# Optimization experiments

Hardware: AMD Instinct MI355X
Metric: run time of the kernel (lower is better)

Reference implementation:

```python
import jax, jax.numpy as jnp
import numpy as np

B, N, D = 2, 2048, 1024
CTX, TV = 256, 250
H, DH = 16, 64
INNER = H * DH          # 1024
FF = 4 * D              # 4096 (GEGLU inner)
SCALE = DH ** -0.5


def _layernorm(x, g, b):
    mu = x.mean(-1, keepdims=True)
    var = ((x - mu) ** 2).mean(-1, keepdims=True)
    return (x - mu) / jnp.sqrt(var + 1e-5) * g + b


def _attn(xq, ctx, wq, wk, wv, wo, bo):
    b, n, _ = xq.shape
    m = ctx.shape[1]
    q = (xq @ wq).reshape(b, n, H, DH)
    k = (ctx @ wk).reshape(b, m, H, DH)
    v = (ctx @ wv).reshape(b, m, H, DH)
    sim = jnp.einsum('bihd,bjhd->bhij', q, k) * SCALE
    att = jax.nn.softmax(sim, axis=-1)
    out = jnp.einsum('bhij,bjhd->bihd', att, v).reshape(b, n, INNER)
    return out @ wo + bo


def _sin_pe(T, d):
    pos = jnp.arange(T, dtype=jnp.float32)[:, None]
    den = jnp.power(10000.0, 2.0 * jnp.arange(d // 2, dtype=jnp.float32) / d)
    ang = pos / den                                  # [T, d/2]
    return jnp.stack([jnp.sin(ang), jnp.cos(ang)], -1).reshape(T, d)


def setup_inputs() -> dict:
    key = jax.random.key(0)
    ks = jax.random.split(key, 40)
    w = lambda k, s: jax.random.normal(k, s, jnp.float32) * 0.02
    inp = {
        'x': jax.random.normal(ks[0], (B, N, D), jnp.float32),
        'context': jax.random.normal(ks[1], (B, CTX, D), jnp.float32),
        'hint_control': jax.random.normal(ks[2], (B, TV, D), jnp.float32),
        'ln1_g': jnp.ones((D,)), 'ln1_b': jnp.zeros((D,)),
        'ln2_g': jnp.ones((D,)), 'ln2_b': jnp.zeros((D,)),
        'ln3_g': jnp.ones((D,)), 'ln3_b': jnp.zeros((D,)),
        'ln4_g': jnp.ones((D,)), 'ln4_b': jnp.zeros((D,)),
        'a1_wq': w(ks[3], (D, INNER)), 'a1_wk': w(ks[4], (D, INNER)),
        'a1_wv': w(ks[5], (D, INNER)), 'a1_wo': w(ks[6], (INNER, D)),
        'a1_bo': jnp.zeros((D,)),
        'a2_wq': w(ks[7], (D, INNER)), 'a2_wk': w(ks[8], (D, INNER)),
        'a2_wv': w(ks[9], (D, INNER)), 'a2_wo': w(ks[10], (INNER, D)),
        'a2_bo': jnp.zeros((D,)),
        'a3_wq': w(ks[11], (D, INNER)), 'a3_wk': w(ks[12], (D, INNER)),
        'a3_wv': w(ks[13], (D, INNER)), 'a3_wo': w(ks[14], (INNER, D)),
        'a3_bo': jnp.zeros((D,)),
        'ff_w1': w(ks[15], (D, 2 * FF)), 'ff_b1': jnp.zeros((2 * FF,)),
        'ff_w2': w(ks[16], (FF, D)), 'ff_b2': jnp.zeros((D,)),
    }
    return inp


def reference(x, context, hint_control,
              ln1_g, ln1_b, ln2_g, ln2_b, ln3_g, ln3_b, ln4_g, ln4_b,
              a1_wq, a1_wk, a1_wv, a1_wo, a1_bo,
              a2_wq, a2_wk, a2_wv, a2_wo, a2_bo,
              a3_wq, a3_wk, a3_wv, a3_wo, a3_bo,
              ff_w1, ff_b1, ff_w2, ff_b2):
    # attn1: self-attention (disable_self_attn=False -> context is x itself)
    h = _layernorm(x, ln1_g, ln1_b)
    x = _attn(h, h, a1_wq, a1_wk, a1_wv, a1_wo, a1_bo) + x
    # attn2: cross-attention over context
    h = _layernorm(x, ln2_g, ln2_b)
    x = _attn(h, context, a2_wq, a2_wk, a2_wv, a2_wo, a2_bo) + x
    # attn3: video cross-attention with sinusoidal PE added to hint_control
    hint = hint_control + _sin_pe(hint_control.shape[1], D)[None]
    h = _layernorm(x, ln4_g, ln4_b)
    x = _attn(h, hint, a3_wq, a3_wk, a3_wv, a3_wo, a3_bo) + x
    # GEGLU feed-forward
    h = _layernorm(x, ln3_g, ln3_b)
    proj = h @ ff_w1 + ff_b1
    a, gate = jnp.split(proj, 2, axis=-1)
    x = (a * jax.nn.gelu(gate, approximate=False)) @ ff_w2 + ff_b2 + x
    return x
```

## Files before the change

kernel.cpp:

```cpp
#include <hip/hip_runtime.h>
#include <cstdint>

typedef unsigned short u16;
typedef __bf16 bf16x8 __attribute__((ext_vector_type(8)));
typedef float f32x4 __attribute__((ext_vector_type(4)));

__device__ __forceinline__ u16 f2bf(float f) {
  union { float f; uint32_t u; } x; x.f = f;
  uint32_t r = x.u + 0x7FFFu + ((x.u >> 16) & 1u);
  return (u16)(r >> 16);
}
__device__ __forceinline__ bf16x8 ld8s(const u16* p) {
  return *reinterpret_cast<const bf16x8*>(p);
}
__device__ __forceinline__ float geluf(float x) {
  return 0.5f * x * (1.f + erff(x * 0.70710678118654752f));
}
__device__ __forceinline__ uint32_t cvtpk(float a, float b) {
  uint32_t r;
  asm("v_cvt_pk_bf16_f32 %0, %1, %2" : "=v"(r) : "v"(a), "v"(b));
  return r;
}
__device__ __forceinline__ void gload16(const u16* g, u16* l) {
  __builtin_amdgcn_global_load_lds(
      (__attribute__((address_space(1))) void*)const_cast<u16*>(g),
      (__attribute__((address_space(3))) void*)l, 16, 0, 0);
}

struct PrepJob {
  const void* src; void* dst;
  int K, N, mode, row_off, ldo, s_lo, s_hi, blk0;
};
struct PrepArgs { PrepJob j[17]; };

__global__ __launch_bounds__(256) void wprep_kernel(PrepArgs a) {
  __shared__ float tile[32][33];
  int bid = blockIdx.x;
  int t = threadIdx.x;
  const float* src = nullptr; void* dst = nullptr;
  int K = 0, N = 0, mode = 0, roff = 0, ldo = 0, slo = 0, shi = 0, bl = 0;
#pragma unroll
  for (int i = 0; i < 17; ++i) {
    int lo = a.j[i].blk0;
    int hi = (i == 16) ? 0x7fffffff : a.j[i + 1].blk0;
    if (bid >= lo && bid < hi) {
      src = (const float*)a.j[i].src; dst = a.j[i].dst;
      K = a.j[i].K; N = a.j[i].N; mode = a.j[i].mode; roff = a.j[i].row_off;
      ldo = a.j[i].ldo; slo = a.j[i].s_lo; shi = a.j[i].s_hi; bl = bid - lo;
    }
  }
  (void)K;
  if (mode <= 1) {
    int nb = N >> 5;
    int bx = bl % nb, by = bl / nb;
    int tx = t & 31, ty = t >> 5;
    int n = bx * 32 + tx, kbase = by * 32;
#pragma unroll
    for (int r = 0; r < 4; ++r)
      tile[ty + r * 8][tx] = src[(size_t)(kbase + ty + r * 8) * N + n];
    __syncthreads();
#pragma unroll
    for (int r = 0; r < 4; ++r) {
      int nl = ty + r * 8, ng = bx * 32 + nl;
      int orow;
      if (mode == 0) orow = roff + ng;
      else {
        if (ng < 4096) orow = ((ng >> 4) << 5) + (ng & 15);
        else { int t2 = ng - 4096; orow = ((t2 >> 4) << 5) + 16 + (t2 & 15); }
      }
      float v = tile[tx][nl];
      if (mode == 0 && orow >= slo && orow < shi) v *= 0.18033688011112042f;
      ((u16*)dst)[(size_t)orow * ldo + kbase + tx] = f2bf(v);
    }
  } else if (mode == 2) {
    int idx = bl * 1024 + t * 4;
    float4 v = *reinterpret_cast<const float4*>(src + idx);
    ushort4 o;
    o.x = f2bf(v.x); o.y = f2bf(v.y); o.z = f2bf(v.z); o.w = f2bf(v.w);
    *reinterpret_cast<ushort4*>((u16*)dst + idx) = o;
  } else if (mode == 3) {
    int row = bl;
    int tt = row % 250;
    int d0 = t * 4;
    int i0 = d0 >> 1;
    float den0 = powf(10000.f, (float)i0 / 512.f);
    float den1 = powf(10000.f, (float)(i0 + 1) / 512.f);
    float a0 = (float)tt / den0, a1 = (float)tt / den1;
    const float* hp = src + (size_t)row * 1024 + d0;
    u16* op = (u16*)dst + (size_t)row * 1024 + d0;
    op[0] = f2bf(hp[0] + sinf(a0));
    op[1] = f2bf(hp[1] + cosf(a0));
    op[2] = f2bf(hp[2] + sinf(a1));
    op[3] = f2bf(hp[3] + cosf(a1));
  } else {
    int i2 = bl * 256 + t;
    int g = i2 >> 5, s2 = i2 & 31;
    int c2 = (s2 < 16) ? (g * 16 + s2) : (4096 + g * 16 + (s2 - 16));
    ((float*)dst)[i2] = src[c2];
  }
}

__global__ __launch_bounds__(256) void ln_kernel(const float* __restrict__ x,
                                                 const float* __restrict__ g,
                                                 const float* __restrict__ b,
                                                 u16* __restrict__ out) {
  int row = blockIdx.x;
  int tid = threadIdx.x;
  int l = tid & 63, w = tid >> 6;
  const float4 v = reinterpret_cast<const float4*>(x + (size_t)row * 1024)[tid];
  float s = v.x + v.y + v.z + v.w;
#pragma unroll
  for (int d = 1; d < 64; d <<= 1) s += __shfl_xor(s, d, 64);
  __shared__ float red[8];
  if (l == 0) red[w] = s;
  __syncthreads();
  float mean = (red[0] + red[1] + red[2] + red[3]) * (1.f / 1024.f);
  float dx = v.x - mean, dy = v.y - mean, dz = v.z - mean, dw = v.w - mean;
  float vs = dx * dx + dy * dy + dz * dz + dw * dw;
#pragma unroll
  for (int d = 1; d < 64; d <<= 1) vs += __shfl_xor(vs, d, 64);
  if (l == 0) red[4 + w] = vs;
  __syncthreads();
  float var = (red[4] + red[5] + red[6] + red[7]) * (1.f / 1024.f);
  float rstd = rsqrtf(var + 1e-5f);
  const float4 g4 = reinterpret_cast<const float4*>(g)[tid];
  const float4 b4 = reinterpret_cast<const float4*>(b)[tid];
  ushort4 o;
  o.x = f2bf(dx * rstd * g4.x + b4.x);
  o.y = f2bf(dy * rstd * g4.y + b4.y);
  o.z = f2bf(dz * rstd * g4.z + b4.z);
  o.w = f2bf(dw * rstd * g4.w + b4.w);
  reinterpret_cast<ushort4*>(out + (size_t)row * 1024)[tid] = o;
}

template <int EPI, bool GUARD>
__global__ __launch_bounds__(256) void gemm_bt_kernel(
    const u16* __restrict__ A, int lda, const u16* __restrict__ Bt,
    void* __restrict__ Cv, int ldc, const float* __restrict__ bias,
    const float* __restrict__ res, int M, int N, int K) {
  __shared__ __align__(16) u16 As[128 * 64];
  __shared__ __align__(16) u16 Bs[128 * 64];
  int t = threadIdx.x;
  int l = t & 63, w = t >> 6;
  int wm = w >> 1, wn = w & 1;
  int lr = l & 15, lg = l >> 4;
  int gx = gridDim.x;
  int nwg = gx * gridDim.y;
  int orig = blockIdx.y * gx + blockIdx.x;
  int qq = nwg >> 3, rr = nwg & 7;
  int xcd = orig & 7, lin = orig >> 3;
  int wg = (xcd < rr ? xcd * (qq + 1) : rr * (qq + 1) + (xcd - rr) * qq) + lin;
  int bx = wg % gx, by = wg / gx;
  int row0 = by * 128, n0 = bx * 128;

  int lrow8 = l >> 3, lchunk = l & 7;
  f32x4 acc[4][4];
#pragma unroll
  for (int i = 0; i < 4; ++i)
#pragma unroll
    for (int j = 0; j < 4; ++j) acc[i][j] = f32x4{0.f, 0.f, 0.f, 0.f};

  int keyA = lr & 7;
  for (int k0 = 0; k0 < K; k0 += 64) {
#pragma unroll
    for (int q = 0; q < 4; ++q) {
      int rbase = w * 32 + q * 8;
      int r = rbase + lrow8;
      int csrc = (lchunk ^ lrow8) * 8;
      int ga = row0 + r;
      if (GUARD) { if (ga > M - 1) ga = M - 1; }
      gload16(&A[(size_t)ga * lda + k0 + csrc], &As[rbase * 64]);
      int gb = n0 + r;
      gload16(&Bt[(size_t)gb * K + k0 + csrc], &Bs[rbase * 64]);
    }
    __syncthreads();
#pragma unroll
    for (int kk = 0; kk < 2; ++kk) {
      bf16x8 af[4], bfv[4];
#pragma unroll
      for (int mi = 0; mi < 4; ++mi)
        af[mi] = ld8s(&As[(wm * 64 + mi * 16 + lr) * 64 + ((((kk << 2) + lg) ^ keyA) << 3)]);
#pragma unroll
      for (int ni = 0; ni < 4; ++ni)
        bfv[ni] = ld8s(&Bs[(wn * 64 + ni * 16 + lr) * 64 + ((((kk << 2) + lg) ^ keyA) << 3)]);
#pragma unroll
      for (int mi = 0; mi < 4; ++mi)
#pragma unroll
        for (int ni = 0; ni < 4; ++ni)
          acc[mi][ni] = __builtin_amdgcn_mfma_f32_16x16x32_bf16(af[mi], bfv[ni], acc[mi][ni], 0, 0, 0);
    }
    __syncthreads();
  }

#pragma unroll
  for (int mi = 0; mi < 4; ++mi) {
    int rowb = row0 + wm * 64 + mi * 16 + lg * 4;
    if (EPI == 2) {
#pragma unroll
      for (int p = 0; p < 2; ++p) {
        int colA = n0 + wn * 64 + p * 32 + lr;
        int colG = colA + 16;
        int ocol = ((n0 + wn * 64) >> 1) + p * 16 + lr;
#pragma unroll
        for (int r = 0; r < 4; ++r) {
          int grow = rowb + r;
          float av = acc[mi][2 * p][r] + bias[colA];
          float gv = acc[mi][2 * p + 1][r] + bias[colG];
          ((u16*)Cv)[(size_t)grow * ldc + ocol] = f2bf(av * geluf(gv));
        }
      }
    } else {
#pragma unroll
      for (int ni = 0; ni < 4; ++ni) {
        int gcol = n0 + wn * 64 + ni * 16 + lr;
#pragma unroll
        for (int r = 0; r < 4; ++r) {
          int grow = rowb + r;
          if (GUARD && grow >= M) continue;
          float v = acc[mi][ni][r];
          if (EPI == 0)
            ((u16*)Cv)[(size_t)grow * ldc + gcol] = f2bf(v);
          else
            ((float*)Cv)[(size_t)grow * ldc + gcol] =
                v + bias[gcol] + res[(size_t)grow * ldc + gcol];
        }
      }
    }
  }
}

template <bool TG>
__global__ __launch_bounds__(256) void attn_kernel(
    const u16* __restrict__ Q, int qs, int qoff,
    const u16* __restrict__ KV, int kvs, int koff, int voff,
    int m, u16* __restrict__ O) {
  int b = blockIdx.z, h = blockIdx.y;
  int t = threadIdx.x;
  int l = t & 63, w = t >> 6;
  int lr = l & 15, lg = l >> 4;
  int q0 = blockIdx.x * 128 + w * 16;
  __shared__ __align__(16) u16 Ks[2][64 * 64];
  __shared__ __align__(16) u16 Vt[2][64 * 64];
  __shared__ __align__(16) u16 Pl[4][16 * 64];

  const u16* qrowA = Q + (size_t)((b << 11) + q0 + lr) * qs + qoff + h * 64;
  const u16* qrowB = qrowA + (size_t)64 * qs;
  bf16x8 qa0 = ld8s(qrowA + lg * 8), qa1 = ld8s(qrowA + 32 + lg * 8);
  bf16x8 qb0 = ld8s(qrowB + lg * 8), qb1 = ld8s(qrowB + 32 + lg * 8);

  f32x4 oA[4], oB[4];
  float psA = 0.f, psB = 0.f;
#pragma unroll
  for (int r = 0; r < 4; ++r) { oA[r] = f32x4{0.f, 0.f, 0.f, 0.f}; oB[r] = f32x4{0.f, 0.f, 0.f, 0.f}; }

  const u16* kvb = KV + (size_t)b * m * kvs + h * 64;
  int kj = t >> 3, kc = t & 7;
  int srcsw = ((l & 7) ^ (l >> 3)) << 3;
  int psw = (lr & 7) ^ ((lr & 8) >> 1);

  {
#pragma unroll
    for (int q2 = 0; q2 < 2; ++q2) {
      int gr = w * 16 + q2 * 8 + (l >> 3);
      if (TG) { if (gr > m - 1) gr = m - 1; }
      gload16(kvb + (size_t)gr * kvs + koff + srcsw, &Ks[0][(w * 16 + q2 * 8) * 64]);
    }
    int jv = kj * 2;
    int gv0 = jv, gv1 = jv + 1;
    if (TG) { if (gv0 > m - 1) gv0 = m - 1; if (gv1 > m - 1) gv1 = m - 1; }
    uint4 va = *reinterpret_cast<const uint4*>(kvb + (size_t)gv0 * kvs + voff + kc * 8);
    uint4 vb2 = *reinterpret_cast<const uint4*>(kvb + (size_t)gv1 * kvs + voff + kc * 8);
    const u16* vap = reinterpret_cast<const u16*>(&va);
    const u16* vbp = reinterpret_cast<const u16*>(&vb2);
    int jb = jv >> 3, jlow = jv & 7;
#pragma unroll
    for (int i = 0; i < 8; ++i) {
      int d = kc * 8 + i;
      int key = (d ^ (d >> 3)) & 7;
      uint32_t pk = (uint32_t)vap[i] | ((uint32_t)vbp[i] << 16);
      *reinterpret_cast<uint32_t*>(&Vt[0][d * 64 + ((jb ^ key) << 3) + jlow]) = pk;
    }
  }
  __syncthreads();

  int nj = (m + 63) >> 6;
  int cur = 0;
  for (int jt = 0; jt < nj; ++jt) {
    int j0 = jt << 6;
    bool hn = (jt + 1 < nj);
    uint4 va, vb2;
    if (hn) {
      int j0n = j0 + 64;
#pragma unroll
      for (int q2 = 0; q2 < 2; ++q2) {
        int gr = j0n + w * 16 + q2 * 8 + (l >> 3);
        if (TG) { if (gr > m - 1) gr = m - 1; }
        gload16(kvb + (size_t)gr * kvs + koff + srcsw, &Ks[cur ^ 1][(w * 16 + q2 * 8) * 64]);
      }
      int jv = kj * 2;
      int gv0 = j0n + jv, gv1 = j0n + jv + 1;
      if (TG) { if (gv0 > m - 1) gv0 = m - 1; if (gv1 > m - 1) gv1 = m - 1; }
      va = *reinterpret_cast<const uint4*>(kvb + (size_t)gv0 * kvs + voff + kc * 8);
      vb2 = *reinterpret_cast<const uint4*>(kvb + (size_t)gv1 * kvs + voff + kc * 8);
    }

    const u16* Kb = Ks[cur];
    f32x4 sA[4], sB[4];
#pragma unroll
    for (int c = 0; c < 4; ++c) {
      sA[c] = f32x4{0.f, 0.f, 0.f, 0.f};
      sB[c] = f32x4{0.f, 0.f, 0.f, 0.f};
      bf16x8 k0 = ld8s(&Kb[(c * 16 + lr) * 64 + ((lg ^ (lr & 7)) << 3)]);
      bf16x8 k1 = ld8s(&Kb[(c * 16 + lr) * 64 + (((4 + lg) ^ (lr & 7)) << 3)]);
      sA[c] = __builtin_amdgcn_mfma_f32_16x16x32_bf16(k0, qa0, sA[c], 0, 0, 0);
      sA[c] = __builtin_amdgcn_mfma_f32_16x16x32_bf16(k1, qa1, sA[c], 0, 0, 0);
      sB[c] = __builtin_amdgcn_mfma_f32_16x16x32_bf16(k0, qb0, sB[c], 0, 0, 0);
      sB[c] = __builtin_amdgcn_mfma_f32_16x16x32_bf16(k1, qb1, sB[c], 0, 0, 0);
    }

    if (hn) {
      const u16* vap = reinterpret_cast<const u16*>(&va);
      const u16* vbp = reinterpret_cast<const u16*>(&vb2);
      int jv = kj * 2;
      int jb = jv >> 3, jlow = jv & 7;
#pragma unroll
      for (int i = 0; i < 8; ++i) {
        int d = kc * 8 + i;
        int key = (d ^ (d >> 3)) & 7;
        uint32_t pk = (uint32_t)vap[i] | ((uint32_t)vbp[i] << 16);
        *reinterpret_cast<uint32_t*>(&Vt[cur ^ 1][d * 64 + ((jb ^ key) << 3) + jlow]) = pk;
      }
    }

    bool tail = TG && (j0 + 64 > m);
    const u16* Vb = Vt[cur];
    bf16x8 vfr[2][4];

    {
      uint32_t pk[8];
#pragma unroll
      for (int c = 0; c < 4; ++c) {
        float p[4];
#pragma unroll
        for (int r = 0; r < 4; ++r) {
          float v = exp2f(sA[c][r]);
          if (tail && (j0 + c * 16 + lg * 4 + r >= m)) v = 0.f;
          p[r] = v; psA += v;
        }
        pk[2 * c] = cvtpk(p[0], p[1]);
        pk[2 * c + 1] = cvtpk(p[2], p[3]);
      }
#pragma unroll
      for (int c = 0; c < 4; ++c) {
        int phys = (2 * c + (lg >> 1)) ^ psw;
        uint2 u; u.x = pk[2 * c]; u.y = pk[2 * c + 1];
        *reinterpret_cast<uint2*>(&Pl[w][lr * 64 + (phys << 3) + ((lg & 1) << 2)]) = u;
      }
#pragma unroll
      for (int ks = 0; ks < 2; ++ks) {
        int physp = (ks * 4 + lg) ^ psw;
        bf16x8 pb = ld8s(&Pl[w][lr * 64 + (physp << 3)]);
#pragma unroll
        for (int dt = 0; dt < 4; ++dt) {
          int d = dt * 16 + lr;
          int key = (d ^ (d >> 3)) & 7;
          vfr[ks][dt] = ld8s(&Vb[d * 64 + ((((ks << 2) + lg) ^ key) << 3)]);
          oA[dt] = __builtin_amdgcn_mfma_f32_16x16x32_bf16(vfr[ks][dt], pb, oA[dt], 0, 0, 0);
        }
      }
    }
    {
      uint32_t pk[8];
#pragma unroll
      for (int c = 0; c < 4; ++c) {
        float p[4];
#pragma unroll
        for (int r = 0; r < 4; ++r) {
          float v = exp2f(sB[c][r]);
          if (tail && (j0 + c * 16 + lg * 4 + r >= m)) v = 0.f;
          p[r] = v; psB += v;
        }
        pk[2 * c] = cvtpk(p[0], p[1]);
        pk[2 * c + 1] = cvtpk(p[2], p[3]);
      }
#pragma unroll
      for (int c = 0; c < 4; ++c) {
        int phys = (2 * c + (lg >> 1)) ^ psw;
        uint2 u; u.x = pk[2 * c]; u.y = pk[2 * c + 1];
        *reinterpret_cast<uint2*>(&Pl[w][lr * 64 + (phys << 3) + ((lg & 1) << 2)]) = u;
      }
#pragma unroll
      for (int ks = 0; ks < 2; ++ks) {
        int physp = (ks * 4 + lg) ^ psw;
        bf16x8 pb = ld8s(&Pl[w][lr * 64 + (physp << 3)]);
#pragma unroll
        for (int dt = 0; dt < 4; ++dt)
          oB[dt] = __builtin_amdgcn_mfma_f32_16x16x32_bf16(vfr[ks][dt], pb, oB[dt], 0, 0, 0);
      }
    }
    __syncthreads();
    cur ^= 1;
  }

  psA += __shfl_xor(psA, 16, 64); psA += __shfl_xor(psA, 32, 64);
  psB += __shfl_xor(psB, 16, 64); psB += __shfl_xor(psB, 32, 64);
  float invA = 1.f / psA, invB = 1.f / psB;
  {
    int grow = (b << 11) + q0 + lr;
    u16* op = O + (size_t)grow * 1024 + h * 64 + lg * 4;
#pragma unroll
    for (int dt = 0; dt < 4; ++dt) {
      uint2 u;
      u.x = cvtpk(oA[dt][0] * invA, oA[dt][1] * invA);
      u.y = cvtpk(oA[dt][2] * invA, oA[dt][3] * invA);
      *reinterpret_cast<uint2*>(op + dt * 16) = u;
    }
    u16* op2 = op + (size_t)64 * 1024;
#pragma unroll
    for (int dt = 0; dt < 4; ++dt) {
      uint2 u;
      u.x = cvtpk(oB[dt][0] * invB, oB[dt][1] * invB);
      u.y = cvtpk(oB[dt][2] * invB, oB[dt][3] * invB);
      *reinterpret_cast<uint2*>(op2 + dt * 16) = u;
    }
  }
}

extern "C" void kernel_launch(void* const* d_in, const int* in_sizes, int n_in,
                              void* d_out, int out_size, void* d_ws, size_t ws_size,
                              hipStream_t stream) {
  const float* x_in = (const float*)d_in[0];
  const float* ctx_in = (const float*)d_in[1];
  const float* hint_in = (const float*)d_in[2];
  const float* ln1g = (const float*)d_in[3]; const float* ln1b = (const float*)d_in[4];
  const float* ln2g = (const float*)d_in[5]; const float* ln2b = (const float*)d_in[6];
  const float* ln3g = (const float*)d_in[7]; const float* ln3b = (const float*)d_in[8];
  const float* ln4g = (const float*)d_in[9]; const float* ln4b = (const float*)d_in[10];
  const float* a1wq = (const float*)d_in[11]; const float* a1wk = (const float*)d_in[12];
  const float* a1wv = (const float*)d_in[13]; const float* a1wo = (const float*)d_in[14];
  const float* a1bo = (const float*)d_in[15];
  const float* a2wq = (const float*)d_in[16]; const float* a2wk = (const float*)d_in[17];
  const float* a2wv = (const float*)d_in[18]; const float* a2wo = (const float*)d_in[19];
  const float* a2bo = (const float*)d_in[20];
  const float* a3wq = (const float*)d_in[21]; const float* a3wk = (const float*)d_in[22];
  const float* a3wv = (const float*)d_in[23]; const float* a3wo = (const float*)d_in[24];
  const float* a3bo = (const float*)d_in[25];
  const float* ffw1 = (const float*)d_in[26]; const float* ffb1 = (const float*)d_in[27];
  const float* ffw2 = (const float*)d_in[28]; const float* ffb2 = (const float*)d_in[29];

  char* wsb = (char*)d_ws;
  size_t off = 0;
  auto alloc = [&](size_t bytes) -> void* {
    void* p = wsb + off;
    off += (bytes + 255) & ~(size_t)255;
    return p;
  };
  u16* wqkv1t = (u16*)alloc(3072ull * 1024 * 2);
  u16* wo1t = (u16*)alloc(1024ull * 1024 * 2);
  u16* wq2t = (u16*)alloc(1024ull * 1024 * 2);
  u16* wkv2t = (u16*)alloc(2048ull * 1024 * 2);
  u16* wo2t = (u16*)alloc(1024ull * 1024 * 2);
  u16* wq3t = (u16*)alloc(1024ull * 1024 * 2);
  u16* wkv3t = (u16*)alloc(2048ull * 1024 * 2);
  u16* wo3t = (u16*)alloc(1024ull * 1024 * 2);
  u16* w1t = (u16*)alloc(8192ull * 1024 * 2);
  u16* w2t = (u16*)alloc(1024ull * 4096 * 2);
  float* b1p = (float*)alloc(8192ull * 4);
  u16* hintbf = (u16*)alloc(500ull * 1024 * 2);
  u16* ctxbf = (u16*)alloc(512ull * 1024 * 2);
  float* xbuf = (float*)alloc(4096ull * 1024 * 4);
  u16* hbf = (u16*)alloc(4096ull * 1024 * 2);
  u16* attnout = (u16*)alloc(4096ull * 1024 * 2);
  u16* qbuf = (u16*)alloc(4096ull * 1024 * 2);
  u16* kvbuf = (u16*)alloc(512ull * 2048 * 2);
  u16* qkv = (u16*)alloc(4096ull * 4096 * 2);
  u16* gbuf = qkv;

  PrepArgs pa;
  int bi = 0, bc = 0;
  auto addJ = [&](const void* s, void* d, int K, int N, int mode, int roff,
                  int ldo, int slo, int shi, int nblk) {
    pa.j[bi].src = s; pa.j[bi].dst = d; pa.j[bi].K = K; pa.j[bi].N = N;
    pa.j[bi].mode = mode; pa.j[bi].row_off = roff; pa.j[bi].ldo = ldo;
    pa.j[bi].s_lo = slo; pa.j[bi].s_hi = shi; pa.j[bi].blk0 = bc;
    bc += nblk; ++bi;
  };
  addJ(a1wq, wqkv1t, 1024, 1024, 0, 0, 1024, 0, 1024, 1024);
  addJ(a1wk, wqkv1t, 1024, 1024, 0, 1024, 1024, 0, 0, 1024);
  addJ(a1wv, wqkv1t, 1024, 1024, 0, 2048, 1024, 0, 0, 1024);
  addJ(a1wo, wo1t, 1024, 1024, 0, 0, 1024, 0, 0, 1024);
  addJ(a2wq, wq2t, 1024, 1024, 0, 0, 1024, 0, 1024, 1024);
  addJ(a2wk, wkv2t, 1024, 1024, 0, 0, 1024, 0, 0, 1024);
  addJ(a2wv, wkv2t, 1024, 1024, 0, 1024, 1024, 0, 0, 1024);
  addJ(a2wo, wo2t, 1024, 1024, 0, 0, 1024, 0, 0, 1024);
  addJ(a3wq, wq3t, 1024, 1024, 0, 0, 1024, 0, 1024, 1024);
  addJ(a3wk, wkv3t, 1024, 1024, 0, 0, 1024, 0, 0, 1024);
  addJ(a3wv, wkv3t, 1024, 1024, 0, 1024, 1024, 0, 0, 1024);
  addJ(a3wo, wo3t, 1024, 1024, 0, 0, 1024, 0, 0, 1024);
  addJ(ffw1, w1t, 1024, 8192, 1, 0, 1024, 0, 0, 8192);
  addJ(ffw2, w2t, 4096, 1024, 0, 0, 4096, 0, 0, 4096);
  addJ(ctx_in, ctxbf, 0, 0, 2, 0, 0, 0, 0, 512);
  addJ(hint_in, hintbf, 0, 0, 3, 0, 0, 0, 0, 500);
  addJ(ffb1, b1p, 0, 0, 4, 0, 0, 0, 0, 32);
  wprep_kernel<<<bc, 256, 0, stream>>>(pa);

  ln_kernel<<<4096, 256, 0, stream>>>(x_in, ln1g, ln1b, hbf);
  gemm_bt_kernel<0, false><<<dim3(24, 32), 256, 0, stream>>>(hbf, 1024, wqkv1t, qkv, 3072,
                                                             nullptr, nullptr, 4096, 3072, 1024);
  attn_kernel<false><<<dim3(16, 16, 2), 256, 0, stream>>>(qkv, 3072, 0, qkv, 3072, 1024, 2048,
                                                          2048, attnout);
  gemm_bt_kernel<1, false><<<dim3(8, 32), 256, 0, stream>>>(attnout, 1024, wo1t, xbuf, 1024,
                                                            a1bo, x_in, 4096, 1024, 1024);

  ln_kernel<<<4096, 256, 0, stream>>>(xbuf, ln2g, ln2b, hbf);
  gemm_bt_kernel<0, false><<<dim3(8, 32), 256, 0, stream>>>(hbf, 1024, wq2t, qbuf, 1024,
                                                            nullptr, nullptr, 4096, 1024, 1024);
  gemm_bt_kernel<0, false><<<dim3(16, 4), 256, 0, stream>>>(ctxbf, 1024, wkv2t, kvbuf, 2048,
                                                            nullptr, nullptr, 512, 2048, 1024);
  attn_kernel<false><<<dim3(16, 16, 2), 256, 0, stream>>>(qbuf, 1024, 0, kvbuf, 2048, 0, 1024,
                                                          256, attnout);
  gemm_bt_kernel<1, false><<<dim3(8, 32), 256, 0, stream>>>(attnout, 1024, wo2t, xbuf, 1024,
                                                            a2bo, xbuf, 4096, 1024, 1024);

  ln_kernel<<<4096, 256, 0, stream>>>(xbuf, ln4g, ln4b, hbf);
  gemm_bt_kernel<0, false><<<dim3(8, 32), 256, 0, stream>>>(hbf, 1024, wq3t, qbuf, 1024,
                                                            nullptr, nullptr, 4096, 1024, 1024);
  gemm_bt_kernel<0, true><<<dim3(16, 4), 256, 0, stream>>>(hintbf, 1024, wkv3t, kvbuf, 2048,
                                                           nullptr, nullptr, 500, 2048, 1024);
  attn_kernel<true><<<dim3(16, 16, 2), 256, 0, stream>>>(qbuf, 1024, 0, kvbuf, 2048, 0, 1024,
                                                         250, attnout);
  gemm_bt_kernel<1, false><<<dim3(8, 32), 256, 0, stream>>>(attnout, 1024, wo3t, xbuf, 1024,
                                                            a3bo, xbuf, 4096, 1024, 1024);

  ln_kernel<<<4096, 256, 0, stream>>>(xbuf, ln3g, ln3b, hbf);
  gemm_bt_kernel<2, false><<<dim3(64, 32), 256, 0, stream>>>(hbf, 1024, w1t, gbuf, 4096,
                                                             b1p, nullptr, 4096, 8192, 1024);
  gemm_bt_kernel<1, false><<<dim3(8, 32), 256, 0, stream>>>(gbuf, 4096, w2t, d_out, 1024,
                                                            ffb2, xbuf, 4096, 1024, 4096);
}
```

Baseline: 548.8 us.

## Add 256x256 double-buffered GEMM kernel for QKV and GEGLU projections

Introduces a new 512-thread GEMM kernel with 256x256 output tiles and double-buffered LDS staging. It replaces the 128x128 kernel for the two largest GEMMs, the fused QKV projection and the GEGLU up-projection. The larger tile raises arithmetic intensity per global load, and the double buffering overlaps the next tile's loads with MFMA work. The cost is 128 KB of LDS per block and heavy register pressure from 32 accumulators per thread, which may limit occupancy. QKV also becomes only 192 blocks, which can underfill the GPU.

```diff
diff --git a/kernel.cpp b/kernel.cpp
--- a/kernel.cpp
+++ b/kernel.cpp
@@ -131,6 +131,101 @@
   o.z = f2bf(dz * rstd * g4.z + b4.z);
   o.w = f2bf(dw * rstd * g4.w + b4.w);
   reinterpret_cast<ushort4*>(out + (size_t)row * 1024)[tid] = o;
+}
+
+template <int EPI>
+__global__ __launch_bounds__(512, 2) void gemm256_kernel(
+    const u16* __restrict__ A, int lda, const u16* __restrict__ Bt,
+    void* __restrict__ Cv, int ldc, const float* __restrict__ bias,
+    int M, int N, int K) {
+  __shared__ __align__(16) u16 As[2][256 * 64];
+  __shared__ __align__(16) u16 Bs[2][256 * 64];
+  int t = threadIdx.x;
+  int l = t & 63, w = t >> 6;
+  int wm = w >> 2, wn = w & 3;
+  int lr = l & 15, lg = l >> 4;
+  int gx = gridDim.x;
+  int nwg = gx * gridDim.y;
+  int orig = blockIdx.y * gx + blockIdx.x;
+  int qq = nwg >> 3, rr = nwg & 7;
+  int xcd = orig & 7, lin = orig >> 3;
+  int wg = (xcd < rr ? xcd * (qq + 1) : rr * (qq + 1) + (xcd - rr) * qq) + lin;
+  int bx = wg % gx, by = wg / gx;
+  int row0 = by * 256, n0 = bx * 256;
+
+  int lrow8 = l >> 3, lchunk = l & 7;
+  int csrc = (lchunk ^ lrow8) * 8;
+  int keyA = lr & 7;
+
+  f32x4 acc[8][4];
+#pragma unroll
+  for (int i = 0; i < 8; ++i)
+#pragma unroll
+    for (int j = 0; j < 4; ++j) acc[i][j] = f32x4{0.f, 0.f, 0.f, 0.f};
+
+  auto stage = [&](int buf, int k0) {
+#pragma unroll
+    for (int q = 0; q < 4; ++q) {
+      int rbase = w * 32 + q * 8;
+      int r = rbase + lrow8;
+      gload16(&A[(size_t)(row0 + r) * lda + k0 + csrc], &As[buf][rbase * 64]);
+      gload16(&Bt[(size_t)(n0 + r) * K + k0 + csrc], &Bs[buf][rbase * 64]);
+    }
+  };
+
+  int nk = K >> 6;
+  stage(0, 0);
+  __syncthreads();
+  int cur = 0;
+  for (int ti = 0; ti < nk; ++ti) {
+    if (ti + 1 < nk) stage(cur ^ 1, (ti + 1) << 6);
+#pragma unroll
+    for (int kk = 0; kk < 2; ++kk) {
+      int chunk = (((kk << 2) + lg) ^ keyA) << 3;
+      bf16x8 af[8];
+#pragma unroll
+      for (int mi = 0; mi < 8; ++mi)
+        af[mi] = ld8s(&As[cur][(wm * 128 + mi * 16 + lr) * 64 + chunk]);
+      bf16x8 bfv[4];
+#pragma unroll
+      for (int ni = 0; ni < 4; ++ni)
+        bfv[ni] = ld8s(&Bs[cur][(wn * 64 + ni * 16 + lr) * 64 + chunk]);
+#pragma unroll
+      for (int mi = 0; mi < 8; ++mi)
+#pragma unroll
+        for (int ni = 0; ni < 4; ++ni)
+          acc[mi][ni] = __builtin_amdgcn_mfma_f32_16x16x32_bf16(af[mi], bfv[ni], acc[mi][ni], 0, 0, 0);
+    }
+    __syncthreads();
+    cur ^= 1;
+  }
+
+#pragma unroll
+  for (int mi = 0; mi < 8; ++mi) {
+    int rowb = row0 + wm * 128 + mi * 16 + lg * 4;
+    if (EPI == 2) {
+#pragma unroll
+      for (int p = 0; p < 2; ++p) {
+        int colA = n0 + wn * 64 + p * 32 + lr;
+        int colG = colA + 16;
+        int ocol = ((n0 + wn * 64) >> 1) + p * 16 + lr;
+#pragma unroll
+        for (int r = 0; r < 4; ++r) {
+          float av = acc[mi][2 * p][r] + bias[colA];
+          float gv = acc[mi][2 * p + 1][r] + bias[colG];
+          ((u16*)Cv)[(size_t)(rowb + r) * ldc + ocol] = f2bf(av * geluf(gv));
+        }
+      }
+    } else {
+#pragma unroll
+      for (int ni = 0; ni < 4; ++ni) {
+        int gcol = n0 + wn * 64 + ni * 16 + lr;
+#pragma unroll
+        for (int r = 0; r < 4; ++r)
+          ((u16*)Cv)[(size_t)(rowb + r) * ldc + gcol] = f2bf(acc[mi][ni][r]);
+      }
+    }
+  }
 }
 
 template <int EPI, bool GUARD>
@@ -505,8 +600,8 @@
   wprep_kernel<<<bc, 256, 0, stream>>>(pa);
 
   ln_kernel<<<4096, 256, 0, stream>>>(x_in, ln1g, ln1b, hbf);
-  gemm_bt_kernel<0, false><<<dim3(24, 32), 256, 0, stream>>>(hbf, 1024, wqkv1t, qkv, 3072,
-                                                             nullptr, nullptr, 4096, 3072, 1024);
+  gemm256_kernel<0><<<dim3(12, 16), 512, 0, stream>>>(hbf, 1024, wqkv1t, qkv, 3072,
+                                                      nullptr, 4096, 3072, 1024);
   attn_kernel<false><<<dim3(16, 16, 2), 256, 0, stream>>>(qkv, 3072, 0, qkv, 3072, 1024, 2048,
                                                           2048, attnout);
   gemm_bt_kernel<1, false><<<dim3(8, 32), 256, 0, stream>>>(attnout, 1024, wo1t, xbuf, 1024,
@@ -533,8 +628,8 @@
                                                             a3bo, xbuf, 4096, 1024, 1024);
 
   ln_kernel<<<4096, 256, 0, stream>>>(xbuf, ln3g, ln3b, hbf);
-  gemm_bt_kernel<2, false><<<dim3(64, 32), 256, 0, stream>>>(hbf, 1024, w1t, gbuf, 4096,
-                                                             b1p, nullptr, 4096, 8192, 1024);
+  gemm256_kernel<2><<<dim3(32, 16), 512, 0, stream>>>(hbf, 1024, w1t, gbuf, 4096,
+                                                      b1p, 4096, 8192, 1024);
   gemm_bt_kernel<1, false><<<dim3(8, 32), 256, 0, stream>>>(gbuf, 4096, w2t, d_out, 1024,
                                                             ffb2, xbuf, 4096, 1024, 4096);
 }
```

Measured after the change: 532.9 us. -2.9%, faster.
